# Kernel tuning notes

Hardware: AMD Instinct MI355X
Metric: run time of the kernel (lower is better)

The kernel has to match this reference:

```python
import jax, jax.numpy as jnp
import numpy as np

N_NODES = 50000
N_EDGES = 800000
N_GRAPHS = 128
D = 128
L = 4
C = 10
GN_EPS = 1e-5


def setup_inputs() -> dict:
    key = jax.random.key(0)
    ks = jax.random.split(key, 12)
    s = 0.05
    x = jax.random.normal(ks[0], (N_NODES, D), dtype=jnp.float32)
    gin_w1 = jax.random.normal(ks[1], (L, D, D), dtype=jnp.float32) * s
    gin_b1 = jax.random.normal(ks[2], (L, D), dtype=jnp.float32) * s
    gin_w2 = jax.random.normal(ks[3], (L, D, D), dtype=jnp.float32) * s
    gin_b2 = jax.random.normal(ks[4], (L, D), dtype=jnp.float32) * s
    gn_weight = jnp.ones((L, D), dtype=jnp.float32)
    gn_bias = jnp.zeros((L, D), dtype=jnp.float32)
    gn_scale = jnp.ones((L, D), dtype=jnp.float32)
    fw1 = jax.random.normal(ks[5], (D, D), dtype=jnp.float32) * s
    fb1 = jnp.zeros((D,), dtype=jnp.float32)
    fw2 = jax.random.normal(ks[6], (D, D), dtype=jnp.float32) * s
    fb2 = jnp.zeros((D,), dtype=jnp.float32)
    fw3 = jax.random.normal(ks[7], (D, C), dtype=jnp.float32) * s
    fb3 = jnp.zeros((C,), dtype=jnp.float32)
    edge_index = jax.random.randint(ks[8], (2, N_EDGES), 0, N_NODES, dtype=jnp.int64)
    batch = jnp.sort(jax.random.randint(ks[9], (N_NODES,), 0, N_GRAPHS, dtype=jnp.int64))
    return dict(x=x, gin_w1=gin_w1, gin_b1=gin_b1, gin_w2=gin_w2, gin_b2=gin_b2,
                gn_weight=gn_weight, gn_bias=gn_bias, gn_scale=gn_scale,
                fw1=fw1, fb1=fb1, fw2=fw2, fb2=fb2, fw3=fw3, fb3=fb3,
                edge_index=edge_index, batch=batch)


def _graph_norm(h, batch, weight, bias, mean_scale, counts):
    # PyG GraphNorm: per-graph mean/var with learnable mean_scale.
    mean = jax.ops.segment_sum(h, batch, num_segments=N_GRAPHS) / counts  # [G, D]
    out = h - mean[batch] * mean_scale
    var = jax.ops.segment_sum(out * out, batch, num_segments=N_GRAPHS) / counts
    return weight * out / jnp.sqrt(var[batch] + GN_EPS) + bias


def reference(x, gin_w1, gin_b1, gin_w2, gin_b2, gn_weight, gn_bias, gn_scale,
              fw1, fb1, fw2, fb2, fw3, fb3, edge_index, batch):
    src, dst = edge_index[0], edge_index[1]
    ones = jnp.ones((N_NODES, 1), dtype=x.dtype)
    counts = jnp.maximum(jax.ops.segment_sum(ones, batch, num_segments=N_GRAPHS), 1.0)  # [G,1]
    h = x
    for l in range(L):
        # GINConv, eps=0: (1+eps)*x + sum_{j->i} x_j, then MLP with act after each Linear
        agg = jax.ops.segment_sum(h[src], dst, num_segments=N_NODES)  # [N, D]
        h = h + agg
        h = jax.nn.relu(h @ gin_w1[l] + gin_b1[l])
        h = jax.nn.relu(h @ gin_w2[l] + gin_b2[l])
        h = _graph_norm(h, batch, gn_weight[l], gn_bias[l], gn_scale[l], counts)
        h = jax.nn.relu(h)
    # sum readout per graph
    g = jax.ops.segment_sum(h, batch, num_segments=N_GRAPHS)  # [G, D]
    # final MLP (dropout is identity in eval)
    g = jax.nn.relu(g @ fw1 + fb1)
    g = jax.nn.relu(g @ fw2 + fb2)
    out = g @ fw3 + fb3
    return jax.nn.log_softmax(out, axis=-1)
```

## Files before the change

### kernel.cpp

```cpp
#include <hip/hip_runtime.h>
#include <cstddef>

#define N_NODES 50000
#define N_EDGES 800000
#define N_GRAPHS 128
#define DIM 128
#define N_LAYERS 4
#define GN_EPS 1e-5f

#define B_CHUNK 256
#define EPB 3125
#define BUCKET_SHIFT 9
#define BUCKET_SIZE 512
#define NB 98

#define CX_BLKS 12500
#define CW_BLKS 512
#define GB_BLKS 196
#define SETUP_BLKS (CX_BLKS + CW_BLKS + GB_BLKS + B_CHUNK)

#define MM_BLKS 391

typedef unsigned short ushort_t;
typedef __attribute__((ext_vector_type(8))) short frag8;
typedef __attribute__((ext_vector_type(4))) float f32x4;

__device__ inline float bfbits2f(unsigned hi16) { return __uint_as_float(hi16 << 16); }
__device__ inline ushort_t bf16rne(float v) {
    unsigned u = __float_as_uint(v);
    unsigned r = u + 0x7fff + ((u >> 16) & 1);
    return (ushort_t)(r >> 16);
}
__device__ inline unsigned packbf2(float a, float b) {
    return (unsigned)bf16rne(a) | ((unsigned)bf16rne(b) << 16);
}
__device__ inline void bf16split(float v, ushort_t& h, ushort_t& l) {
    ushort_t hi = bf16rne(v);
    float fh = __uint_as_float(((unsigned)hi) << 16);
    l = bf16rne(v - fh);
    h = hi;
}

__global__ __launch_bounds__(256) void setup_misc(const float* __restrict__ x, unsigned* __restrict__ Hb,
                                                  const float* __restrict__ w1, const float* __restrict__ w2,
                                                  ushort_t* __restrict__ whi, ushort_t* __restrict__ wlo,
                                                  const int* __restrict__ batch, int* __restrict__ gstart,
                                                  const int* __restrict__ edst, int* __restrict__ cnts) {
    __shared__ int cnt[NB];
    int b = blockIdx.x, t = threadIdx.x;
    if (b < CX_BLKS) {
        int i = b * 256 + t;
        if (i < N_NODES * 64) {
            float a = x[2 * i], bb = x[2 * i + 1];
            Hb[i] = packbf2(a, bb);
        }
    } else if (b < CX_BLKS + CW_BLKS) {
        int idx = (b - CX_BLKS) * 256 + t;
        int mat = idx >> 14;
        int e = idx & 16383;
        int n = e >> 7, k = e & 127;
        int l = mat >> 1;
        const float* src = (mat & 1) ? (w2 + (size_t)l * DIM * DIM) : (w1 + (size_t)l * DIM * DIM);
        float v = src[k * DIM + n];
        ushort_t h, lw;
        bf16split(v, h, lw);
        whi[(size_t)mat * DIM * DIM + n * DIM + k] = h;
        wlo[(size_t)mat * DIM * DIM + n * DIM + k] = lw;
    } else if (b < CX_BLKS + CW_BLKS + GB_BLKS) {
        int i = (b - CX_BLKS - CW_BLKS) * 256 + t;
        if (i < N_NODES) {
            int bb = batch[i];
            if (i == 0) {
                for (int g = 0; g <= bb; ++g) gstart[g] = 0;
            } else {
                int pb = batch[i - 1];
                for (int g = pb + 1; g <= bb; ++g) gstart[g] = i;
            }
            if (i == N_NODES - 1) {
                for (int g = bb + 1; g <= N_GRAPHS; ++g) gstart[g] = N_NODES;
            }
        }
    } else {
        int blk = b - (CX_BLKS + CW_BLKS + GB_BLKS);
        for (int i = t; i < NB; i += 256) cnt[i] = 0;
        __syncthreads();
        int base = blk * EPB;
        for (int i = t; i < EPB; i += 256) atomicAdd(&cnt[edst[base + i] >> BUCKET_SHIFT], 1);
        __syncthreads();
        for (int i = t; i < NB; i += 256) cnts[i * B_CHUNK + blk] = cnt[i];
    }
}

__global__ __launch_bounds__(1024) void scan_local(const int* __restrict__ in, int* __restrict__ out,
                                                   int* __restrict__ bsum, int n) {
    __shared__ int wsum[16];
    int tid = threadIdx.x, lane = tid & 63, w = tid >> 6;
    int gi = blockIdx.x * 1024 + tid;
    int v = (gi < n) ? in[gi] : 0;
    int s = v;
    #pragma unroll
    for (int off = 1; off < 64; off <<= 1) {
        int t = __shfl_up(s, off, 64);
        if (lane >= off) s += t;
    }
    if (lane == 63) wsum[w] = s;
    __syncthreads();
    if (w == 0) {
        int ws = (lane < 16) ? wsum[lane] : 0;
        #pragma unroll
        for (int off = 1; off < 16; off <<= 1) {
            int t = __shfl_up(ws, off, 64);
            if (lane >= off) ws += t;
        }
        if (lane < 16) wsum[lane] = ws;
    }
    __syncthreads();
    int woff = (w > 0) ? wsum[w - 1] : 0;
    if (gi < n) out[gi] = woff + s - v;
    if (tid == 1023) bsum[blockIdx.x] = woff + s;
}

__global__ __launch_bounds__(1024) void scan_add(int* __restrict__ out, const int* __restrict__ bsum,
                                                 int n, int total) {
    int lane = threadIdx.x & 63;
    int v = (lane < (int)blockIdx.x) ? bsum[lane] : 0;
    #pragma unroll
    for (int off = 1; off < 64; off <<= 1) v += __shfl_xor(v, off, 64);
    int gi = blockIdx.x * 1024 + threadIdx.x;
    if (gi < n) out[gi] += v;
    if (blockIdx.x == 0 && threadIdx.x == 0) out[n] = total;
}

__global__ __launch_bounds__(256) void p3_place(const int* __restrict__ src, const int* __restrict__ dst,
                                                const int* __restrict__ off, unsigned* __restrict__ ebuf) {
    __shared__ int cur[NB];
    int t = threadIdx.x, blk = blockIdx.x;
    for (int i = t; i < NB; i += 256) cur[i] = off[i * B_CHUNK + blk];
    __syncthreads();
    int base = blk * EPB;
    for (int i = t; i < EPB; i += 256) {
        int d = dst[base + i];
        int b = d >> BUCKET_SHIFT;
        int pos = atomicAdd(&cur[b], 1);
        ebuf[pos] = (unsigned)src[base + i] | ((unsigned)(d & (BUCKET_SIZE - 1)) << 16);
    }
}

__global__ __launch_bounds__(512) void p4_csr(const unsigned* __restrict__ ebuf, const int* __restrict__ off,
                                              int* __restrict__ eoff, int* __restrict__ csr) {
    __shared__ int cnt[BUCKET_SIZE];
    __shared__ int wsum[8];
    int k = blockIdx.x, t = threadIdx.x;
    int bstart = off[k * B_CHUNK];
    int bend = off[(k + 1) * B_CHUNK];
    cnt[t] = 0;
    __syncthreads();
    for (int i = bstart + t; i < bend; i += 512) atomicAdd(&cnt[ebuf[i] >> 16], 1);
    __syncthreads();
    int lane = t & 63, w = t >> 6;
    int v = cnt[t], s = v;
    #pragma unroll
    for (int o = 1; o < 64; o <<= 1) {
        int tt = __shfl_up(s, o, 64);
        if (lane >= o) s += tt;
    }
    if (lane == 63) wsum[w] = s;
    __syncthreads();
    if (w == 0) {
        int ws = (lane < 8) ? wsum[lane] : 0;
        #pragma unroll
        for (int o = 1; o < 8; o <<= 1) {
            int tt = __shfl_up(ws, o, 64);
            if (lane >= o) ws += tt;
        }
        if (lane < 8) wsum[lane] = ws;
    }
    __syncthreads();
    int woff = (w > 0) ? wsum[w - 1] : 0;
    int excl = woff + s - v;
    int node = k * BUCKET_SIZE + t;
    if (node < N_NODES) eoff[node] = bstart + excl;
    __syncthreads();
    cnt[t] = excl;
    __syncthreads();
    for (int i = bstart + t; i < bend; i += 512) {
        unsigned p = ebuf[i];
        int pos = atomicAdd(&cnt[p >> 16], 1);
        csr[bstart + pos] = (int)(p & 0xffffu);
    }
    if (k == NB - 1 && t == 0) eoff[N_NODES] = N_EDGES;
}

__global__ __launch_bounds__(512, 4) void mm_fused(const uint4* __restrict__ h4,
                                                   const int* __restrict__ eoff, const int* __restrict__ csr,
                                                   const ushort_t* __restrict__ W1h, const ushort_t* __restrict__ W1l,
                                                   const ushort_t* __restrict__ W2h, const ushort_t* __restrict__ W2l,
                                                   const float* __restrict__ b1, const float* __restrict__ b2,
                                                   ushort_t* __restrict__ Zb) {
    __shared__ ushort_t As[128 * 128];
    __shared__ ushort_t Ws[128 * 128];
    int tid = threadIdx.x;
    int row0 = blockIdx.x * 128;
    int wave = tid >> 6, lane = tid & 63;
    int qtr = lane >> 4, ql = lane & 15;

    for (int i = 0; i < 16; ++i) {
        int r = wave * 16 + i;
        int node = row0 + r;
        float a[8];
        #pragma unroll
        for (int k = 0; k < 8; ++k) a[k] = 0.f;
        auto acc_row = [&](uint4 w) {
            a[0] += bfbits2f(w.x & 0xffffu); a[1] += bfbits2f(w.x >> 16);
            a[2] += bfbits2f(w.y & 0xffffu); a[3] += bfbits2f(w.y >> 16);
            a[4] += bfbits2f(w.z & 0xffffu); a[5] += bfbits2f(w.z >> 16);
            a[6] += bfbits2f(w.w & 0xffffu); a[7] += bfbits2f(w.w >> 16);
        };
        if (node < N_NODES) {
            if (qtr == 0) acc_row(h4[(size_t)node * 16 + ql]);
            int lo = eoff[node], hi = eoff[node + 1];
            for (int base = lo; base < hi; base += 64) {
                int nav = hi - base;
                if (nav > 64) nav = 64;
                int jv = (base + lane < hi) ? csr[base + lane] : 0;
                int cmin = nav >> 2;
                int cmax = (nav + 3) >> 2;
                int ii = 0;
                for (; ii + 3 < cmin; ii += 4) {
                    int j0 = __shfl(jv, 4 * (ii + 0) + qtr, 64);
                    int j1 = __shfl(jv, 4 * (ii + 1) + qtr, 64);
                    int j2 = __shfl(jv, 4 * (ii + 2) + qtr, 64);
                    int j3 = __shfl(jv, 4 * (ii + 3) + qtr, 64);
                    uint4 w0 = h4[(size_t)j0 * 16 + ql];
                    uint4 w1 = h4[(size_t)j1 * 16 + ql];
                    uint4 w2 = h4[(size_t)j2 * 16 + ql];
                    uint4 w3 = h4[(size_t)j3 * 16 + ql];
                    acc_row(w0); acc_row(w1); acc_row(w2); acc_row(w3);
                }
                for (; ii < cmin; ++ii) {
                    int j = __shfl(jv, 4 * ii + qtr, 64);
                    acc_row(h4[(size_t)j * 16 + ql]);
                }
                for (; ii < cmax; ++ii) {
                    int epos = 4 * ii + qtr;
                    int j = __shfl(jv, epos, 64);
                    if (epos < nav) acc_row(h4[(size_t)j * 16 + ql]);
                }
            }
            #pragma unroll
            for (int k = 0; k < 8; ++k) {
                a[k] += __shfl_down(a[k], 32, 64);
                a[k] += __shfl_down(a[k], 16, 64);
            }
        }
        if (qtr == 0) {
            uint4 o;
            o.x = packbf2(a[0], a[1]);
            o.y = packbf2(a[2], a[3]);
            o.z = packbf2(a[4], a[5]);
            o.w = packbf2(a[6], a[7]);
            *(uint4*)(&As[r * 128 + ((ql ^ (r & 7)) * 8)]) = o;
        }
    }

    int q = qtr, mn = ql;
    f32x4 acc[8];
    #pragma unroll
    for (int n = 0; n < 8; ++n) acc[n] = (f32x4)(0.f);

    auto stageW = [&](const ushort_t* src) {
        #pragma unroll
        for (int i = 0; i < 4; ++i) {
            int c = tid + i * 512;
            int r = c >> 4, c8 = c & 15;
            uint4 v = *(const uint4*)(src + r * DIM + c8 * 8);
            *(uint4*)(&Ws[r * 128 + (c8 ^ (r & 7)) * 8]) = v;
        }
    };
    auto compute = [&]() {
        #pragma unroll
        for (int ks = 0; ks < 4; ++ks) {
            int m0 = wave * 16 + mn;
            frag8 a0 = *(const frag8*)&As[m0 * 128 + (((ks * 4 + q) ^ (m0 & 7)) * 8)];
            #pragma unroll
            for (int n = 0; n < 8; ++n) {
                int nr = n * 16 + mn;
                frag8 b = *(const frag8*)&Ws[nr * 128 + (((ks * 4 + q) ^ (nr & 7)) * 8)];
                acc[n] = __builtin_amdgcn_mfma_f32_16x16x32_bf16(a0, b, acc[n], 0, 0, 0);
            }
        }
    };

    stageW(W1h);
    __syncthreads(); compute(); __syncthreads();
    stageW(W1l);
    __syncthreads(); compute(); __syncthreads();

    int mloc = wave * 16;
    #pragma unroll
    for (int n = 0; n < 8; ++n) {
        int col = n * 16 + mn;
        float bv = b1[col];
        #pragma unroll
        for (int r = 0; r < 4; ++r) {
            int rloc = mloc + q * 4 + r;
            float v = fmaxf(acc[n][r] + bv, 0.f);
            As[rloc * 128 + ((col >> 3) ^ (rloc & 7)) * 8 + (col & 7)] = bf16rne(v);
            acc[n][r] = 0.f;
        }
    }
    __syncthreads();
    stageW(W2h);
    __syncthreads(); compute(); __syncthreads();
    stageW(W2l);
    __syncthreads(); compute();

    #pragma unroll
    for (int n = 0; n < 8; ++n) {
        int col = n * 16 + mn;
        float bv = b2[col];
        #pragma unroll
        for (int r = 0; r < 4; ++r) {
            int grow = row0 + mloc + q * 4 + r;
            if (grow < N_NODES)
                Zb[(size_t)grow * DIM + col] = bf16rne(fmaxf(acc[n][r] + bv, 0.f));
        }
    }
}

__global__ __launch_bounds__(1024) void gn_fused(const unsigned* __restrict__ Zb, const int* __restrict__ gstart,
                                                 const float* __restrict__ scale, const float* __restrict__ weight,
                                                 const float* __restrict__ bias,
                                                 unsigned* __restrict__ Hb) {
    __shared__ f32x4 sh1[1024], sh2[1024];
    __shared__ float sa[64], sb[64];
    int g = blockIdx.x >> 1, half = blockIdx.x & 1;
    int t = threadIdx.x;
    int uld = t & 15, rg = t >> 4;
    int s = gstart[g], e = gstart[g + 1];
    const unsigned* zp = Zb + half * 32 + uld * 2;
    f32x4 s1 = (f32x4)(0.f), s2 = (f32x4)(0.f);
    for (int n = s + rg; n < e; n += 64) {
        uint2 zz = *(const uint2*)(zp + (size_t)n * 64);
        f32x4 z;
        z[0] = bfbits2f(zz.x & 0xffffu); z[1] = bfbits2f(zz.x >> 16);
        z[2] = bfbits2f(zz.y & 0xffffu); z[3] = bfbits2f(zz.y >> 16);
        s1 += z;
        s2 += z * z;
    }
    sh1[t] = s1;
    sh2[t] = s2;
    __syncthreads();
    int dbase = half * 64 + uld * 4;
    if (rg == 0) {
        #pragma unroll 8
        for (int k = 1; k < 64; ++k) { s1 += sh1[uld + 16 * k]; s2 += sh2[uld + 16 * k]; }
        int cnt = e - s;
        float cf = (float)(cnt > 0 ? cnt : 1);
        #pragma unroll
        for (int j = 0; j < 4; ++j) {
            float m = s1[j] / cf, ez = s2[j] / cf;
            float sc = scale[dbase + j];
            float var = fmaxf(ez - (2.0f - sc) * sc * m * m, 0.f);
            sa[uld * 4 + j] = m * sc;
            sb[uld * 4 + j] = weight[dbase + j] / sqrtf(var + GN_EPS);
        }
    }
    __syncthreads();
    float as0 = sa[uld * 4], as1 = sa[uld * 4 + 1], as2 = sa[uld * 4 + 2], as3 = sa[uld * 4 + 3];
    float bm0 = sb[uld * 4], bm1 = sb[uld * 4 + 1], bm2 = sb[uld * 4 + 2], bm3 = sb[uld * 4 + 3];
    float bi0 = bias[dbase], bi1 = bias[dbase + 1], bi2 = bias[dbase + 2], bi3 = bias[dbase + 3];
    unsigned* hp = Hb + half * 32 + uld * 2;
    for (int n = s + rg; n < e; n += 64) {
        uint2 zz = *(const uint2*)(zp + (size_t)n * 64);
        float z0 = bfbits2f(zz.x & 0xffffu), z1 = bfbits2f(zz.x >> 16);
        float z2 = bfbits2f(zz.y & 0xffffu), z3 = bfbits2f(zz.y >> 16);
        float o0 = fmaxf((z0 - as0) * bm0 + bi0, 0.f);
        float o1 = fmaxf((z1 - as1) * bm1 + bi1, 0.f);
        float o2 = fmaxf((z2 - as2) * bm2 + bi2, 0.f);
        float o3 = fmaxf((z3 - as3) * bm3 + bi3, 0.f);
        uint2 o;
        o.x = packbf2(o0, o1);
        o.y = packbf2(o2, o3);
        *(uint2*)(hp + (size_t)n * 64) = o;
    }
}

__global__ __launch_bounds__(1024) void gn_last(const unsigned* __restrict__ Zb, const int* __restrict__ gstart,
                                                const float* __restrict__ scale, const float* __restrict__ weight,
                                                const float* __restrict__ bias,
                                                const float* __restrict__ fw1, const float* __restrict__ fb1,
                                                const float* __restrict__ fw2, const float* __restrict__ fb2,
                                                const float* __restrict__ fw3, const float* __restrict__ fb3,
                                                float* __restrict__ out) {
    __shared__ f32x4 sh1[1024], sh2[1024];
    __shared__ float sa[128], sb[128];
    __shared__ float v0[128], v1[128], v2[128], lg[10];
    int g = blockIdx.x;
    int t = threadIdx.x;
    int du = t & 31, rg = t >> 5;
    int s = gstart[g], e = gstart[g + 1];
    const unsigned* zp = Zb + du * 2;
    f32x4 s1 = (f32x4)(0.f), s2 = (f32x4)(0.f);
    for (int n = s + rg; n < e; n += 32) {
        uint2 zz = *(const uint2*)(zp + (size_t)n * 64);
        f32x4 z;
        z[0] = bfbits2f(zz.x & 0xffffu); z[1] = bfbits2f(zz.x >> 16);
        z[2] = bfbits2f(zz.y & 0xffffu); z[3] = bfbits2f(zz.y >> 16);
        s1 += z;
        s2 += z * z;
    }
    sh1[t] = s1;
    sh2[t] = s2;
    __syncthreads();
    int dbase = du * 4;
    if (rg == 0) {
        #pragma unroll 8
        for (int k = 1; k < 32; ++k) { s1 += sh1[du + 32 * k]; s2 += sh2[du + 32 * k]; }
        int cnt = e - s;
        float cf = (float)(cnt > 0 ? cnt : 1);
        #pragma unroll
        for (int j = 0; j < 4; ++j) {
            float m = s1[j] / cf, ez = s2[j] / cf;
            float sc = scale[dbase + j];
            float var = fmaxf(ez - (2.0f - sc) * sc * m * m, 0.f);
            sa[dbase + j] = m * sc;
            sb[dbase + j] = weight[dbase + j] / sqrtf(var + GN_EPS);
        }
    }
    __syncthreads();
    float as_[4], bm_[4], bi_[4];
    #pragma unroll
    for (int j = 0; j < 4; ++j) {
        as_[j] = sa[dbase + j];
        bm_[j] = sb[dbase + j];
        bi_[j] = bias[dbase + j];
    }
    f32x4 rsum = (f32x4)(0.f);
    for (int n = s + rg; n < e; n += 32) {
        uint2 zz = *(const uint2*)(zp + (size_t)n * 64);
        float z0 = bfbits2f(zz.x & 0xffffu), z1 = bfbits2f(zz.x >> 16);
        float z2 = bfbits2f(zz.y & 0xffffu), z3 = bfbits2f(zz.y >> 16);
        rsum[0] += fmaxf((z0 - as_[0]) * bm_[0] + bi_[0], 0.f);
        rsum[1] += fmaxf((z1 - as_[1]) * bm_[1] + bi_[1], 0.f);
        rsum[2] += fmaxf((z2 - as_[2]) * bm_[2] + bi_[2], 0.f);
        rsum[3] += fmaxf((z3 - as_[3]) * bm_[3] + bi_[3], 0.f);
    }
    __syncthreads();
    sh1[t] = rsum;
    __syncthreads();
    if (rg == 0) {
        #pragma unroll 8
        for (int k = 1; k < 32; ++k) rsum += sh1[du + 32 * k];
        #pragma unroll
        for (int j = 0; j < 4; ++j) v0[dbase + j] = rsum[j];
    }
    __syncthreads();
    if (t < 128) {
        float acc = fb1[t];
        for (int d = 0; d < 128; ++d) acc += v0[d] * fw1[d * 128 + t];
        v1[t] = fmaxf(acc, 0.f);
    }
    __syncthreads();
    if (t < 128) {
        float acc = fb2[t];
        for (int d = 0; d < 128; ++d) acc += v1[d] * fw2[d * 128 + t];
        v2[t] = fmaxf(acc, 0.f);
    }
    __syncthreads();
    if (t < 10) {
        float acc = fb3[t];
        for (int d = 0; d < 128; ++d) acc += v2[d] * fw3[d * 10 + t];
        lg[t] = acc;
    }
    __syncthreads();
    if (t < 10) {
        float m = -1e30f;
        for (int c = 0; c < 10; ++c) m = fmaxf(m, lg[c]);
        float ssum = 0.f;
        for (int c = 0; c < 10; ++c) ssum += expf(lg[c] - m);
        out[g * 10 + t] = lg[t] - m - logf(ssum);
    }
}

extern "C" void kernel_launch(void* const* d_in, const int* in_sizes, int n_in,
                              void* d_out, int out_size, void* d_ws, size_t ws_size,
                              hipStream_t stream) {
    const float* x      = (const float*)d_in[0];
    const float* gin_w1 = (const float*)d_in[1];
    const float* gin_b1 = (const float*)d_in[2];
    const float* gin_w2 = (const float*)d_in[3];
    const float* gin_b2 = (const float*)d_in[4];
    const float* gn_w   = (const float*)d_in[5];
    const float* gn_b   = (const float*)d_in[6];
    const float* gn_s   = (const float*)d_in[7];
    const float* fw1    = (const float*)d_in[8];
    const float* fb1    = (const float*)d_in[9];
    const float* fw2    = (const float*)d_in[10];
    const float* fb2    = (const float*)d_in[11];
    const float* fw3    = (const float*)d_in[12];
    const float* fb3    = (const float*)d_in[13];
    const int*   eidx   = (const int*)d_in[14];
    const int*   batch  = (const int*)d_in[15];
    float* out = (float*)d_out;

    const int* esrc = eidx;
    const int* edst = eidx + N_EDGES;

    auto align_up = [](size_t v) { return (v + 255) & ~(size_t)255; };
    char* p = (char*)d_ws;
    unsigned* Hb = (unsigned*)p;   p += align_up((size_t)N_NODES * DIM * 2);
    unsigned* Zb = (unsigned*)p;   p += align_up((size_t)N_NODES * DIM * 2);
    ushort_t* WThi = (ushort_t*)p; p += align_up((size_t)8 * DIM * DIM * 2);
    ushort_t* WTlo = (ushort_t*)p; p += align_up((size_t)8 * DIM * DIM * 2);
    int* gstart = (int*)p;         p += align_up((N_GRAPHS + 1) * 4);
    int* cnts = (int*)p;           p += align_up((size_t)NB * B_CHUNK * 4);
    int* off = (int*)p;            p += align_up(((size_t)NB * B_CHUNK + 1) * 4);
    int* bsum = (int*)p;           p += align_up(64 * 4);
    unsigned* ebuf = (unsigned*)p; p += align_up((size_t)N_EDGES * 4);
    int* eoff = (int*)p;           p += align_up((N_NODES + 1) * 4);
    int* csr = (int*)p;            p += align_up((size_t)N_EDGES * 4);

    const int SCAN_N = NB * B_CHUNK;
    const int SCAN_BLKS = (SCAN_N + 1023) / 1024;
    setup_misc<<<SETUP_BLKS, 256, 0, stream>>>(x, Hb, gin_w1, gin_w2, WThi, WTlo,
                                               batch, gstart, edst, cnts);
    scan_local<<<SCAN_BLKS, 1024, 0, stream>>>(cnts, off, bsum, SCAN_N);
    scan_add<<<SCAN_BLKS, 1024, 0, stream>>>(off, bsum, SCAN_N, N_EDGES);
    p3_place<<<B_CHUNK, 256, 0, stream>>>(esrc, edst, off, ebuf);
    p4_csr<<<NB, 512, 0, stream>>>(ebuf, off, eoff, csr);

    for (int l = 0; l < N_LAYERS; ++l) {
        mm_fused<<<MM_BLKS, 512, 0, stream>>>((const uint4*)Hb, eoff, csr,
            WThi + (size_t)(2 * l) * DIM * DIM, WTlo + (size_t)(2 * l) * DIM * DIM,
            WThi + (size_t)(2 * l + 1) * DIM * DIM, WTlo + (size_t)(2 * l + 1) * DIM * DIM,
            gin_b1 + l * DIM, gin_b2 + l * DIM, (ushort_t*)Zb);
        if (l == N_LAYERS - 1)
            gn_last<<<N_GRAPHS, 1024, 0, stream>>>(Zb, gstart, gn_s + l * DIM,
                gn_w + l * DIM, gn_b + l * DIM, fw1, fb1, fw2, fb2, fw3, fb3, out);
        else
            gn_fused<<<N_GRAPHS * 2, 1024, 0, stream>>>(Zb, gstart, gn_s + l * DIM,
                gn_w + l * DIM, gn_b + l * DIM, Hb);
    }
}
```

Measured before the change: 451.4 us.

## Split neighbor aggregation into separate wave-per-node kernel and widen MLP tiles

Moves the CSR gather-sum out of the fused MLP kernel into a standalone kernel with one wave per node over many blocks, writing bf16 aggregates to a new buffer. The MLP kernel now loads 256-row tiles and computes two 16-row MFMA fragments per wave, reusing each staged weight tile across more rows. The goal is better latency hiding for the irregular gather, which previously ran inside few large blocks. In exchange it adds an intermediate global write/read and an extra launch per layer, and the MLP grid shrinks below the CU count.

Result: faster. 382.4 us (-15.3%).

```diff
diff --git a/kernel.cpp b/kernel.cpp
--- a/kernel.cpp
+++ b/kernel.cpp
@@ -18,8 +18,6 @@
 #define CW_BLKS 512
 #define GB_BLKS 196
 #define SETUP_BLKS (CX_BLKS + CW_BLKS + GB_BLKS + B_CHUNK)
-
-#define MM_BLKS 391
 
 typedef unsigned short ushort_t;
 typedef __attribute__((ext_vector_type(8))) short frag8;
@@ -191,83 +189,99 @@
     if (k == NB - 1 && t == 0) eoff[N_NODES] = N_EDGES;
 }
 
-__global__ __launch_bounds__(512, 4) void mm_fused(const uint4* __restrict__ h4,
-                                                   const int* __restrict__ eoff, const int* __restrict__ csr,
-                                                   const ushort_t* __restrict__ W1h, const ushort_t* __restrict__ W1l,
-                                                   const ushort_t* __restrict__ W2h, const ushort_t* __restrict__ W2l,
-                                                   const float* __restrict__ b1, const float* __restrict__ b2,
-                                                   ushort_t* __restrict__ Zb) {
-    __shared__ ushort_t As[128 * 128];
+__global__ __launch_bounds__(256) void agg_bf16(const uint4* __restrict__ h4, const int* __restrict__ eoff,
+                                                const int* __restrict__ csr, uint4* __restrict__ T4) {
+    int wid = (blockIdx.x * 256 + threadIdx.x) >> 6;
+    int lane = threadIdx.x & 63;
+    int qtr = lane >> 4;
+    int ql = lane & 15;
+    if (wid >= N_NODES) return;
+    int lo = eoff[wid], hi = eoff[wid + 1];
+
+    float a[8];
+    #pragma unroll
+    for (int k = 0; k < 8; ++k) a[k] = 0.f;
+
+    auto acc_row = [&](uint4 w) {
+        a[0] += bfbits2f(w.x & 0xffffu); a[1] += bfbits2f(w.x >> 16);
+        a[2] += bfbits2f(w.y & 0xffffu); a[3] += bfbits2f(w.y >> 16);
+        a[4] += bfbits2f(w.z & 0xffffu); a[5] += bfbits2f(w.z >> 16);
+        a[6] += bfbits2f(w.w & 0xffffu); a[7] += bfbits2f(w.w >> 16);
+    };
+
+    if (qtr == 0) acc_row(h4[(size_t)wid * 16 + ql]);
+
+    for (int base = lo; base < hi; base += 64) {
+        int nav = hi - base;
+        if (nav > 64) nav = 64;
+        int jv = (base + lane < hi) ? csr[base + lane] : 0;
+        int cmin = nav >> 2;
+        int cmax = (nav + 3) >> 2;
+        int i = 0;
+        for (; i + 3 < cmin; i += 4) {
+            int j0 = __shfl(jv, 4 * (i + 0) + qtr, 64);
+            int j1 = __shfl(jv, 4 * (i + 1) + qtr, 64);
+            int j2 = __shfl(jv, 4 * (i + 2) + qtr, 64);
+            int j3 = __shfl(jv, 4 * (i + 3) + qtr, 64);
+            uint4 w0 = h4[(size_t)j0 * 16 + ql];
+            uint4 w1 = h4[(size_t)j1 * 16 + ql];
+            uint4 w2 = h4[(size_t)j2 * 16 + ql];
+            uint4 w3 = h4[(size_t)j3 * 16 + ql];
+            acc_row(w0); acc_row(w1); acc_row(w2); acc_row(w3);
+        }
+        for (; i < cmin; ++i) {
+            int j = __shfl(jv, 4 * i + qtr, 64);
+            acc_row(h4[(size_t)j * 16 + ql]);
+        }
+        for (; i < cmax; ++i) {
+            int epos = 4 * i + qtr;
+            int j = __shfl(jv, epos, 64);
+            if (epos < nav) acc_row(h4[(size_t)j * 16 + ql]);
+        }
+    }
+
+    #pragma unroll
+    for (int k = 0; k < 8; ++k) {
+        a[k] += __shfl_down(a[k], 32, 64);
+        a[k] += __shfl_down(a[k], 16, 64);
+    }
+    if (qtr == 0) {
+        uint4 o;
+        o.x = packbf2(a[0], a[1]);
+        o.y = packbf2(a[2], a[3]);
+        o.z = packbf2(a[4], a[5]);
+        o.w = packbf2(a[6], a[7]);
+        T4[(size_t)wid * 16 + ql] = o;
+    }
+}
+
+__global__ __launch_bounds__(512) void mm_layer(const ushort_t* __restrict__ A,
+                                                const ushort_t* __restrict__ W1h, const ushort_t* __restrict__ W1l,
+                                                const ushort_t* __restrict__ W2h, const ushort_t* __restrict__ W2l,
+                                                const float* __restrict__ b1, const float* __restrict__ b2,
+                                                ushort_t* __restrict__ Zb) {
+    __shared__ ushort_t As[256 * 128];
     __shared__ ushort_t Ws[128 * 128];
     int tid = threadIdx.x;
-    int row0 = blockIdx.x * 128;
+    int row0 = blockIdx.x * 256;
     int wave = tid >> 6, lane = tid & 63;
-    int qtr = lane >> 4, ql = lane & 15;
-
-    for (int i = 0; i < 16; ++i) {
-        int r = wave * 16 + i;
-        int node = row0 + r;
-        float a[8];
-        #pragma unroll
-        for (int k = 0; k < 8; ++k) a[k] = 0.f;
-        auto acc_row = [&](uint4 w) {
-            a[0] += bfbits2f(w.x & 0xffffu); a[1] += bfbits2f(w.x >> 16);
-            a[2] += bfbits2f(w.y & 0xffffu); a[3] += bfbits2f(w.y >> 16);
-            a[4] += bfbits2f(w.z & 0xffffu); a[5] += bfbits2f(w.z >> 16);
-            a[6] += bfbits2f(w.w & 0xffffu); a[7] += bfbits2f(w.w >> 16);
-        };
-        if (node < N_NODES) {
-            if (qtr == 0) acc_row(h4[(size_t)node * 16 + ql]);
-            int lo = eoff[node], hi = eoff[node + 1];
-            for (int base = lo; base < hi; base += 64) {
-                int nav = hi - base;
-                if (nav > 64) nav = 64;
-                int jv = (base + lane < hi) ? csr[base + lane] : 0;
-                int cmin = nav >> 2;
-                int cmax = (nav + 3) >> 2;
-                int ii = 0;
-                for (; ii + 3 < cmin; ii += 4) {
-                    int j0 = __shfl(jv, 4 * (ii + 0) + qtr, 64);
-                    int j1 = __shfl(jv, 4 * (ii + 1) + qtr, 64);
-                    int j2 = __shfl(jv, 4 * (ii + 2) + qtr, 64);
-                    int j3 = __shfl(jv, 4 * (ii + 3) + qtr, 64);
-                    uint4 w0 = h4[(size_t)j0 * 16 + ql];
-                    uint4 w1 = h4[(size_t)j1 * 16 + ql];
-                    uint4 w2 = h4[(size_t)j2 * 16 + ql];
-                    uint4 w3 = h4[(size_t)j3 * 16 + ql];
-                    acc_row(w0); acc_row(w1); acc_row(w2); acc_row(w3);
-                }
-                for (; ii < cmin; ++ii) {
-                    int j = __shfl(jv, 4 * ii + qtr, 64);
-                    acc_row(h4[(size_t)j * 16 + ql]);
-                }
-                for (; ii < cmax; ++ii) {
-                    int epos = 4 * ii + qtr;
-                    int j = __shfl(jv, epos, 64);
-                    if (epos < nav) acc_row(h4[(size_t)j * 16 + ql]);
-                }
-            }
-            #pragma unroll
-            for (int k = 0; k < 8; ++k) {
-                a[k] += __shfl_down(a[k], 32, 64);
-                a[k] += __shfl_down(a[k], 16, 64);
-            }
-        }
-        if (qtr == 0) {
-            uint4 o;
-            o.x = packbf2(a[0], a[1]);
-            o.y = packbf2(a[2], a[3]);
-            o.z = packbf2(a[4], a[5]);
-            o.w = packbf2(a[6], a[7]);
-            *(uint4*)(&As[r * 128 + ((ql ^ (r & 7)) * 8)]) = o;
-        }
-    }
-
-    int q = qtr, mn = ql;
-    f32x4 acc[8];
-    #pragma unroll
-    for (int n = 0; n < 8; ++n) acc[n] = (f32x4)(0.f);
-
+    int q = lane >> 4, mn = lane & 15;
+
+    f32x4 acc[2][8];
+    #pragma unroll
+    for (int t = 0; t < 2; ++t)
+        #pragma unroll
+        for (int n = 0; n < 8; ++n) acc[t][n] = (f32x4)(0.f);
+
+    #pragma unroll
+    for (int i = 0; i < 8; ++i) {
+        int c = tid + i * 512;
+        int r = c >> 4, c8 = c & 15;
+        uint4 v = make_uint4(0u, 0u, 0u, 0u);
+        int gr = row0 + r;
+        if (gr < N_NODES) v = *(const uint4*)(A + (size_t)gr * DIM + c8 * 8);
+        *(uint4*)(&As[r * 128 + (c8 ^ (r & 7)) * 8]) = v;
+    }
     auto stageW = [&](const ushort_t* src) {
         #pragma unroll
         for (int i = 0; i < 4; ++i) {
@@ -280,13 +294,16 @@
     auto compute = [&]() {
         #pragma unroll
         for (int ks = 0; ks < 4; ++ks) {
-            int m0 = wave * 16 + mn;
+            int m0 = wave * 32 + mn;
+            int m1 = m0 + 16;
             frag8 a0 = *(const frag8*)&As[m0 * 128 + (((ks * 4 + q) ^ (m0 & 7)) * 8)];
+            frag8 a1 = *(const frag8*)&As[m1 * 128 + (((ks * 4 + q) ^ (m1 & 7)) * 8)];
             #pragma unroll
             for (int n = 0; n < 8; ++n) {
                 int nr = n * 16 + mn;
                 frag8 b = *(const frag8*)&Ws[nr * 128 + (((ks * 4 + q) ^ (nr & 7)) * 8)];
-                acc[n] = __builtin_amdgcn_mfma_f32_16x16x32_bf16(a0, b, acc[n], 0, 0, 0);
+                acc[0][n] = __builtin_amdgcn_mfma_f32_16x16x32_bf16(a0, b, acc[0][n], 0, 0, 0);
+                acc[1][n] = __builtin_amdgcn_mfma_f32_16x16x32_bf16(a1, b, acc[1][n], 0, 0, 0);
             }
         }
     };
@@ -296,17 +313,20 @@
     stageW(W1l);
     __syncthreads(); compute(); __syncthreads();
 
-    int mloc = wave * 16;
-    #pragma unroll
-    for (int n = 0; n < 8; ++n) {
-        int col = n * 16 + mn;
-        float bv = b1[col];
-        #pragma unroll
-        for (int r = 0; r < 4; ++r) {
-            int rloc = mloc + q * 4 + r;
-            float v = fmaxf(acc[n][r] + bv, 0.f);
-            As[rloc * 128 + ((col >> 3) ^ (rloc & 7)) * 8 + (col & 7)] = bf16rne(v);
-            acc[n][r] = 0.f;
+    int mloc = wave * 32;
+    #pragma unroll
+    for (int t = 0; t < 2; ++t) {
+        #pragma unroll
+        for (int n = 0; n < 8; ++n) {
+            int col = n * 16 + mn;
+            float bv = b1[col];
+            #pragma unroll
+            for (int r = 0; r < 4; ++r) {
+                int rloc = mloc + t * 16 + q * 4 + r;
+                float v = fmaxf(acc[t][n][r] + bv, 0.f);
+                As[rloc * 128 + ((col >> 3) ^ (rloc & 7)) * 8 + (col & 7)] = bf16rne(v);
+                acc[t][n][r] = 0.f;
+            }
         }
     }
     __syncthreads();
@@ -316,14 +336,17 @@
     __syncthreads(); compute();
 
     #pragma unroll
-    for (int n = 0; n < 8; ++n) {
-        int col = n * 16 + mn;
-        float bv = b2[col];
-        #pragma unroll
-        for (int r = 0; r < 4; ++r) {
-            int grow = row0 + mloc + q * 4 + r;
-            if (grow < N_NODES)
-                Zb[(size_t)grow * DIM + col] = bf16rne(fmaxf(acc[n][r] + bv, 0.f));
+    for (int t = 0; t < 2; ++t) {
+        #pragma unroll
+        for (int n = 0; n < 8; ++n) {
+            int col = n * 16 + mn;
+            float bv = b2[col];
+            #pragma unroll
+            for (int r = 0; r < 4; ++r) {
+                int grow = row0 + mloc + t * 16 + q * 4 + r;
+                if (grow < N_NODES)
+                    Zb[(size_t)grow * DIM + col] = bf16rne(fmaxf(acc[t][n][r] + bv, 0.f));
+            }
         }
     }
 }
@@ -510,6 +533,7 @@
     auto align_up = [](size_t v) { return (v + 255) & ~(size_t)255; };
     char* p = (char*)d_ws;
     unsigned* Hb = (unsigned*)p;   p += align_up((size_t)N_NODES * DIM * 2);
+    unsigned* Tb = (unsigned*)p;   p += align_up((size_t)N_NODES * DIM * 2);
     unsigned* Zb = (unsigned*)p;   p += align_up((size_t)N_NODES * DIM * 2);
     ushort_t* WThi = (ushort_t*)p; p += align_up((size_t)8 * DIM * DIM * 2);
     ushort_t* WTlo = (ushort_t*)p; p += align_up((size_t)8 * DIM * DIM * 2);
@@ -530,8 +554,10 @@
     p3_place<<<B_CHUNK, 256, 0, stream>>>(esrc, edst, off, ebuf);
     p4_csr<<<NB, 512, 0, stream>>>(ebuf, off, eoff, csr);
 
+    const int mm_grid = (N_NODES + 255) / 256;
     for (int l = 0; l < N_LAYERS; ++l) {
-        mm_fused<<<MM_BLKS, 512, 0, stream>>>((const uint4*)Hb, eoff, csr,
+        agg_bf16<<<(N_NODES + 3) / 4, 256, 0, stream>>>((const uint4*)Hb, eoff, csr, (uint4*)Tb);
+        mm_layer<<<mm_grid, 512, 0, stream>>>((const ushort_t*)Tb,
             WThi + (size_t)(2 * l) * DIM * DIM, WTlo + (size_t)(2 * l) * DIM * DIM,
             WThi + (size_t)(2 * l + 1) * DIM * DIM, WTlo + (size_t)(2 * l + 1) * DIM * DIM,
             gin_b1 + l * DIM, gin_b2 + l * DIM, (ushort_t*)Zb);
```
